# Optimization experiments

Measured on AMD Instinct MI355X. Metric: run time of the kernel, lower is better.

The kernel has to match this reference:

```python
import jax, jax.numpy as jnp
import numpy as np

OUT_C, IN_C, KC = 256, 256, 26
KD = 25  # dilated_kernel_size
BATCH, LEN = 32, 1024


def setup_inputs() -> dict:
    key = jax.random.key(0)
    k1, k2, k3, k4 = jax.random.split(key, 4)
    x = jax.random.normal(k1, (BATCH, IN_C, LEN), dtype=jnp.float32)
    # kaiming-uniform-ish weight
    bound = 1.0 / np.sqrt(IN_C * KC)
    weight = jax.random.uniform(k2, (OUT_C, IN_C, KC), minval=-bound, maxval=bound, dtype=jnp.float32)
    # dalean=True: sign shared across out_channels, broadcast
    sign = jnp.broadcast_to(jnp.sign(jax.random.normal(k3, (IN_C, KC), dtype=jnp.float32)), (OUT_C, IN_C, KC))
    lim = KD // 2
    P = jnp.clip(0.5 * jax.random.normal(k4, (1, OUT_C, IN_C, KC), dtype=jnp.float32), -lim, lim)
    SIG = jnp.full((1, OUT_C, IN_C, KC), 0.23, dtype=jnp.float32)  # gauss init
    return {"x": x, "weight": weight, "sign": sign, "P": P, "SIG": SIG}


def _construct_kernel_gauss(W, P, SIG):
    # W: (O,I,C); P,SIG: (1,O,I,C)
    idx = jnp.arange(KD, dtype=W.dtype)[:, None, None, None]       # (KD,1,1,1)
    Pc = P[0] + KD // 2                                            # (O,I,C)
    S = jnp.abs(SIG[0]) + 0.27                                     # (O,I,C)
    X = jnp.exp(-0.5 * ((idx - Pc) / S) ** 2)                      # (KD,O,I,C)
    X = X / (X.sum(0) + 1e-7)                                      # normalize over KD
    K = jnp.einsum('doic,oic->oid', X, W)                          # (O,I,KD)
    return K


def reference(x, weight, sign, P, SIG):
    K = _construct_kernel_gauss(weight * sign, P, SIG)
    # conv1d, stride 1, padding 0, dilation 1, groups 1
    out = jax.lax.conv_general_dilated(
        x, K, window_strides=(1,), padding='VALID',
        dimension_numbers=('NCH', 'OIH', 'NCH'))
    return out  # (BATCH, OUT_C, LEN - KD + 1)
```

## Files before the change

kernel.cpp:

```cpp
#include <hip/hip_runtime.h>
#include <hip/hip_bf16.h>

#define OUT_C 256
#define IN_C  256
#define KC    26
#define KD    25
#define BATCH 32
#define LEN   1024
#define LOUT  (LEN - KD + 1)

#define BM 128
#define BL 128
#define ICH 64
#define NIC (IN_C / ICH)
#define XROWS (BL + KD - 1)
#define SLABSZ (OUT_C * ICH)

typedef short bf16x8 __attribute__((ext_vector_type(8)));
typedef float f32x4  __attribute__((ext_vector_type(4)));

static __device__ __forceinline__ unsigned short f2bf(float f) {
    unsigned int u = __float_as_uint(f);
    u = (u + 0x7FFFu + ((u >> 16) & 1u)) >> 16;
    return (unsigned short)u;
}
static __device__ __forceinline__ float bf2f(unsigned short h) {
    return __uint_as_float(((unsigned int)h) << 16);
}

__global__ __launch_bounds__(256) void build_kernel(
    const float* __restrict__ weight,
    const float* __restrict__ sign,
    const float* __restrict__ P,
    const float* __restrict__ SIG,
    unsigned short* __restrict__ Kh,
    unsigned short* __restrict__ Kl)
{
    int tid = blockIdx.x * blockDim.x + threadIdx.x;
    if (tid >= OUT_C * IN_C) return;
    const int o = tid / IN_C;
    const int i = tid % IN_C;
    const int base = tid * KC;

    float K[KD];
#pragma unroll
    for (int d = 0; d < KD; ++d) K[d] = 0.f;

    for (int c = 0; c < KC; ++c) {
        const float w   = weight[base + c] * sign[base + c];
        const float pc  = P[base + c] + (float)(KD / 2);
        const float s   = fabsf(SIG[base + c]) + 0.27f;
        const float inv = 1.f / s;
        float e[KD];
        float sum = 0.f;
#pragma unroll
        for (int d = 0; d < KD; ++d) {
            const float t = ((float)d - pc) * inv;
            e[d] = __expf(-0.5f * t * t);
            sum += e[d];
        }
        const float wn = w / (sum + 1e-7f);
#pragma unroll
        for (int d = 0; d < KD; ++d) K[d] += wn * e[d];
    }

    const int ic = i >> 6;
    const int il = i & 63;
#pragma unroll
    for (int d = 0; d < KD; ++d) {
        const int off = (d * NIC + ic) * SLABSZ + o * ICH + il;
        const float v = K[d];
        const unsigned short h = f2bf(v);
        const unsigned short l = f2bf(v - bf2f(h));
        Kh[off] = h;
        Kl[off] = l;
    }
}

__global__ __launch_bounds__(256, 2) void conv_kernel(
    const float* __restrict__ x,
    const unsigned short* __restrict__ Kh,
    const unsigned short* __restrict__ Kl,
    float* __restrict__ out)
{
    __shared__ __align__(16) unsigned short xs_h[XROWS * ICH];
    __shared__ __align__(16) unsigned short xs_l[XROWS * ICH];

    const int tid = threadIdx.x;
    const unsigned int Bid = blockIdx.x;
    const int ot = Bid & 1;
    const int lt = (Bid >> 1) & 7;
    const int b  = Bid >> 4;
    const int o0 = ot * BM;
    const int l0 = lt * BL;

    const int lane = tid & 63;
    const int wid  = tid >> 6;
    const int wm   = wid >> 1;
    const int wn   = wid & 1;
    const int n16  = lane & 15;
    const int g    = lane >> 4;

    const int kbase = (o0 + wm * 64 + n16) * ICH + g * 8;

    f32x4 acc[4][4] = {};
    bf16x8 Ah0[4], Al0[4], Ah1[4], Al1[4];

#define LOADA(BUFH, BUFL, SLAB, KT)                                       \
    {                                                                     \
        const int _e0 = (SLAB) * SLABSZ + kbase + (KT) * 32;              \
        _Pragma("unroll")                                                 \
        for (int mt = 0; mt < 4; ++mt) {                                  \
            BUFH[mt] = *(const bf16x8*)&Kh[_e0 + mt * (16 * ICH)];        \
            BUFL[mt] = *(const bf16x8*)&Kl[_e0 + mt * (16 * ICH)];        \
        }                                                                 \
    }

#define COMPUTE(AH, AL, KT, D)                                            \
    {                                                                     \
        bf16x8 bh[4], bl[4];                                              \
        _Pragma("unroll")                                                 \
        for (int nt = 0; nt < 4; ++nt) {                                  \
            const int row  = wn * 64 + nt * 16 + n16 + (D);               \
            const int slot = ((KT) * 4 + g) ^ (row & 7);                  \
            const int pos  = row * ICH + slot * 8;                        \
            bh[nt] = *(const bf16x8*)&xs_h[pos];                          \
            bl[nt] = *(const bf16x8*)&xs_l[pos];                          \
        }                                                                 \
        _Pragma("unroll")                                                 \
        for (int mt = 0; mt < 4; ++mt)                                    \
            _Pragma("unroll")                                             \
            for (int nt = 0; nt < 4; ++nt) {                              \
                acc[mt][nt] = __builtin_amdgcn_mfma_f32_16x16x32_bf16(    \
                    AL[mt], bh[nt], acc[mt][nt], 0, 0, 0);                \
                acc[mt][nt] = __builtin_amdgcn_mfma_f32_16x16x32_bf16(    \
                    AH[mt], bl[nt], acc[mt][nt], 0, 0, 0);                \
                acc[mt][nt] = __builtin_amdgcn_mfma_f32_16x16x32_bf16(    \
                    AH[mt], bh[nt], acc[mt][nt], 0, 0, 0);                \
            }                                                             \
    }

    int slab = 0;
    LOADA(Ah0, Al0, 0, 0);

#pragma unroll 1
    for (int ic = 0; ic < NIC; ++ic) {
        const int xbase = (b * IN_C + ic * ICH) * LEN;
        for (int idx = tid; idx < (ICH / 8) * XROWS; idx += 256) {
            const int c8 = idx / XROWS;
            const int r  = idx - c8 * XROWS;
            const int gl = l0 + r;
            const int ci = c8 * 8;
            float v[8];
#pragma unroll
            for (int j = 0; j < 8; ++j)
                v[j] = (gl < LEN) ? x[xbase + (ci + j) * LEN + gl] : 0.f;
            unsigned int ph[4], pl[4];
#pragma unroll
            for (int j = 0; j < 4; ++j) {
                const unsigned short h0  = f2bf(v[2 * j]);
                const unsigned short h1  = f2bf(v[2 * j + 1]);
                const unsigned short l0s = f2bf(v[2 * j] - bf2f(h0));
                const unsigned short l1s = f2bf(v[2 * j + 1] - bf2f(h1));
                ph[j] = (unsigned int)h0 | ((unsigned int)h1 << 16);
                pl[j] = (unsigned int)l0s | ((unsigned int)l1s << 16);
            }
            const int slot = r * 8 + (c8 ^ (r & 7));
            ((uint4*)xs_h)[slot] = make_uint4(ph[0], ph[1], ph[2], ph[3]);
            ((uint4*)xs_l)[slot] = make_uint4(pl[0], pl[1], pl[2], pl[3]);
        }
        __syncthreads();

#pragma unroll 1
        for (int d = 0; d < KD; ++d) {
            const int slabNext = (d < KD - 1) ? slab + NIC
                               : (ic < NIC - 1 ? ic + 1 : slab);
            LOADA(Ah1, Al1, slab, 1);
            COMPUTE(Ah0, Al0, 0, d);
            LOADA(Ah0, Al0, slabNext, 0);
            COMPUTE(Ah1, Al1, 1, d);
            slab = slabNext;
        }
        __syncthreads();
    }

#undef LOADA
#undef COMPUTE

#pragma unroll
    for (int mt = 0; mt < 4; ++mt)
#pragma unroll
        for (int nt = 0; nt < 4; ++nt) {
            const int l = l0 + wn * 64 + nt * 16 + n16;
            if (l < LOUT) {
#pragma unroll
                for (int r = 0; r < 4; ++r) {
                    const int o = o0 + wm * 64 + mt * 16 + g * 4 + r;
                    out[(b * OUT_C + o) * LOUT + l] = acc[mt][nt][r];
                }
            }
        }
}

extern "C" void kernel_launch(void* const* d_in, const int* in_sizes, int n_in,
                              void* d_out, int out_size, void* d_ws, size_t ws_size,
                              hipStream_t stream)
{
    (void)in_sizes; (void)n_in; (void)out_size; (void)ws_size;

    const float* x      = (const float*)d_in[0];
    const float* weight = (const float*)d_in[1];
    const float* sign   = (const float*)d_in[2];
    const float* P      = (const float*)d_in[3];
    const float* SIG    = (const float*)d_in[4];
    float*       out    = (float*)d_out;

    unsigned short* Kh = (unsigned short*)d_ws;
    unsigned short* Kl = Kh + (size_t)KD * NIC * SLABSZ;

    build_kernel<<<dim3((OUT_C * IN_C + 255) / 256), dim3(256), 0, stream>>>(
        weight, sign, P, SIG, Kh, Kl);

    conv_kernel<<<dim3(512), dim3(256), 0, stream>>>(x, Kh, Kl, out);
}
```

Baseline: 490.5 us.

## Coalesce build_kernel parameter loads via LDS staging and interleave A-fragment prefetch

New measurement: 483.7 us. No clear change (-1.4%).

```diff
diff --git a/kernel.cpp b/kernel.cpp
--- a/kernel.cpp
+++ b/kernel.cpp
@@ -15,6 +15,7 @@
 #define NIC (IN_C / ICH)
 #define XROWS (BL + KD - 1)
 #define SLABSZ (OUT_C * ICH)
+#define CCHUNK 13
 
 typedef short bf16x8 __attribute__((ext_vector_type(8)));
 typedef float f32x4  __attribute__((ext_vector_type(4)));
@@ -36,36 +37,53 @@
     unsigned short* __restrict__ Kh,
     unsigned short* __restrict__ Kl)
 {
-    int tid = blockIdx.x * blockDim.x + threadIdx.x;
-    if (tid >= OUT_C * IN_C) return;
-    const int o = tid / IN_C;
-    const int i = tid % IN_C;
-    const int base = tid * KC;
+    __shared__ float Ws[256 * CCHUNK];
+    __shared__ float Ps[256 * CCHUNK];
+    __shared__ float Ss[256 * CCHUNK];
+
+    const int tid = threadIdx.x;
+    const int o   = blockIdx.x;
+    const int gbase = o * IN_C * KC;
 
     float K[KD];
 #pragma unroll
     for (int d = 0; d < KD; ++d) K[d] = 0.f;
 
-    for (int c = 0; c < KC; ++c) {
-        const float w   = weight[base + c] * sign[base + c];
-        const float pc  = P[base + c] + (float)(KD / 2);
-        const float s   = fabsf(SIG[base + c]) + 0.27f;
-        const float inv = 1.f / s;
-        float e[KD];
-        float sum = 0.f;
-#pragma unroll
-        for (int d = 0; d < KD; ++d) {
-            const float t = ((float)d - pc) * inv;
-            e[d] = __expf(-0.5f * t * t);
-            sum += e[d];
-        }
-        const float wn = w / (sum + 1e-7f);
-#pragma unroll
-        for (int d = 0; d < KD; ++d) K[d] += wn * e[d];
-    }
-
-    const int ic = i >> 6;
-    const int il = i & 63;
+#pragma unroll 1
+    for (int cc = 0; cc < KC; cc += CCHUNK) {
+        __syncthreads();
+        for (int q = tid; q < 256 * CCHUNK; q += 256) {
+            const int p = q / CCHUNK;
+            const int c = q - p * CCHUNK;
+            const int gidx = gbase + p * KC + cc + c;
+            Ws[q] = weight[gidx] * sign[gidx];
+            Ps[q] = P[gidx] + (float)(KD / 2);
+            Ss[q] = fabsf(SIG[gidx]) + 0.27f;
+        }
+        __syncthreads();
+
+#pragma unroll 1
+        for (int c = 0; c < CCHUNK; ++c) {
+            const float w   = Ws[tid * CCHUNK + c];
+            const float pc  = Ps[tid * CCHUNK + c];
+            const float s   = Ss[tid * CCHUNK + c];
+            const float inv = 1.f / s;
+            float e[KD];
+            float sum = 0.f;
+#pragma unroll
+            for (int d = 0; d < KD; ++d) {
+                const float t = ((float)d - pc) * inv;
+                e[d] = __expf(-0.5f * t * t);
+                sum += e[d];
+            }
+            const float wn = w / (sum + 1e-7f);
+#pragma unroll
+            for (int d = 0; d < KD; ++d) K[d] += wn * e[d];
+        }
+    }
+
+    const int ic = tid >> 6;
+    const int il = tid & 63;
 #pragma unroll
     for (int d = 0; d < KD; ++d) {
         const int off = (d * NIC + ic) * SLABSZ + o * ICH + il;
@@ -104,19 +122,16 @@
     const int kbase = (o0 + wm * 64 + n16) * ICH + g * 8;
 
     f32x4 acc[4][4] = {};
-    bf16x8 Ah0[4], Al0[4], Ah1[4], Al1[4];
-
-#define LOADA(BUFH, BUFL, SLAB, KT)                                       \
+    bf16x8 A0h[4], A0l[4], A1h[4], A1l[4];
+
+#define LOAD_MT(BH, BL_, SLAB, KT, MT)                                    \
     {                                                                     \
-        const int _e0 = (SLAB) * SLABSZ + kbase + (KT) * 32;              \
-        _Pragma("unroll")                                                 \
-        for (int mt = 0; mt < 4; ++mt) {                                  \
-            BUFH[mt] = *(const bf16x8*)&Kh[_e0 + mt * (16 * ICH)];        \
-            BUFL[mt] = *(const bf16x8*)&Kl[_e0 + mt * (16 * ICH)];        \
-        }                                                                 \
-    }
-
-#define COMPUTE(AH, AL, KT, D)                                            \
+        const int _e = (SLAB) * SLABSZ + kbase + (KT) * 32 + (MT) * (16 * ICH); \
+        BH[MT]  = *(const bf16x8*)&Kh[_e];                                \
+        BL_[MT] = *(const bf16x8*)&Kl[_e];                                \
+    }
+
+#define PHASE(CH, CL, NH, NL, KT, NSLAB, NKT, D)                          \
     {                                                                     \
         bf16x8 bh[4], bl[4];                                              \
         _Pragma("unroll")                                                 \
@@ -128,20 +143,23 @@
             bl[nt] = *(const bf16x8*)&xs_l[pos];                          \
         }                                                                 \
         _Pragma("unroll")                                                 \
-        for (int mt = 0; mt < 4; ++mt)                                    \
+        for (int mt = 0; mt < 4; ++mt) {                                  \
+            LOAD_MT(NH, NL, NSLAB, NKT, mt);                              \
             _Pragma("unroll")                                             \
             for (int nt = 0; nt < 4; ++nt) {                              \
                 acc[mt][nt] = __builtin_amdgcn_mfma_f32_16x16x32_bf16(    \
-                    AL[mt], bh[nt], acc[mt][nt], 0, 0, 0);                \
+                    CL[mt], bh[nt], acc[mt][nt], 0, 0, 0);                \
                 acc[mt][nt] = __builtin_amdgcn_mfma_f32_16x16x32_bf16(    \
-                    AH[mt], bl[nt], acc[mt][nt], 0, 0, 0);                \
+                    CH[mt], bl[nt], acc[mt][nt], 0, 0, 0);                \
                 acc[mt][nt] = __builtin_amdgcn_mfma_f32_16x16x32_bf16(    \
-                    AH[mt], bh[nt], acc[mt][nt], 0, 0, 0);                \
+                    CH[mt], bh[nt], acc[mt][nt], 0, 0, 0);                \
             }                                                             \
+        }                                                                 \
     }
 
     int slab = 0;
-    LOADA(Ah0, Al0, 0, 0);
+#pragma unroll
+    for (int mt = 0; mt < 4; ++mt) LOAD_MT(A0h, A0l, 0, 0, mt);
 
 #pragma unroll 1
     for (int ic = 0; ic < NIC; ++ic) {
@@ -175,17 +193,15 @@
         for (int d = 0; d < KD; ++d) {
             const int slabNext = (d < KD - 1) ? slab + NIC
                                : (ic < NIC - 1 ? ic + 1 : slab);
-            LOADA(Ah1, Al1, slab, 1);
-            COMPUTE(Ah0, Al0, 0, d);
-            LOADA(Ah0, Al0, slabNext, 0);
-            COMPUTE(Ah1, Al1, 1, d);
+            PHASE(A0h, A0l, A1h, A1l, 0, slab, 1, d);
+            PHASE(A1h, A1l, A0h, A0l, 1, slabNext, 0, d);
             slab = slabNext;
         }
         __syncthreads();
     }
 
-#undef LOADA
-#undef COMPUTE
+#undef LOAD_MT
+#undef PHASE
 
 #pragma unroll
     for (int mt = 0; mt < 4; ++mt)
@@ -218,7 +234,7 @@
     unsigned short* Kh = (unsigned short*)d_ws;
     unsigned short* Kl = Kh + (size_t)KD * NIC * SLABSZ;
 
-    build_kernel<<<dim3((OUT_C * IN_C + 255) / 256), dim3(256), 0, stream>>>(
+    build_kernel<<<dim3(OUT_C), dim3(256), 0, stream>>>(
         weight, sign, P, SIG, Kh, Kl);
 
     conv_kernel<<<dim3(512), dim3(256), 0, stream>>>(x, Kh, Kl, out);
```
